# Kernel tuning notes

Measured on AMD Instinct MI355X. Metric: run time of the kernel, lower is better.

## Reference

```python
import jax, jax.numpy as jnp
import numpy as np
import math

B, T, L, C = 4, 8, 512, 768
H = 8
HD = C // H  # 96
EPS = 1e-12  # F.normalize eps


def _l2norm(x):
    # F.normalize(x, dim=-1): x / max(||x||2, eps)
    n = jnp.sqrt(jnp.sum(x * x, axis=-1, keepdims=True))
    return x / jnp.maximum(n, EPS)


def setup_inputs() -> dict:
    key = jax.random.key(0)
    ks = jax.random.split(key, 7)
    s = 1.0 / math.sqrt(C)
    x = jax.random.normal(ks[0], (B, T, L, C), dtype=jnp.float32)
    Wq = jax.random.uniform(ks[1], (C, C), jnp.float32, -s, s)
    bq = jax.random.uniform(ks[2], (C,), jnp.float32, -s, s)
    Wkv = jax.random.uniform(ks[3], (C, 2 * C), jnp.float32, -s, s)
    bkv = jax.random.uniform(ks[4], (2 * C,), jnp.float32, -s, s)
    Wm = jax.random.uniform(ks[5], (C, C), jnp.float32, -s, s)
    bm = jax.random.uniform(ks[6], (C,), jnp.float32, -s, s)
    return {"x": x, "Wq": Wq, "bq": bq, "Wkv": Wkv, "bkv": bkv, "Wm": Wm, "bm": bm}


def reference(x, Wq, bq, Wkv, bkv, Wm, bm):
    b, t, l, c = x.shape
    # q: (b,t,l,c) -> (b,t,H,l,hd), L2-normalized over hd
    q = (x @ Wq + bq).reshape(b, t, l, H, HD).transpose(0, 1, 3, 2, 4)
    q = _l2norm(q)
    # kv: (b,t,l,2c) -> (b,t,2H,l,hd); chunk on head axis -> k = heads [0,H), v = heads [H,2H)
    kv = (x @ Wkv + bkv).reshape(b, t, l, 2 * H, HD).transpose(0, 1, 3, 2, 4)
    k = _l2norm(kv[:, :, :H])
    v = _l2norm(kv[:, :, H:])
    # attention (dropout on scores is identity in eval mode)
    scores = jnp.einsum("bthqd,bthkd->bthqk", q, k) / math.sqrt(HD)
    attn = jax.nn.softmax(scores, axis=-1)
    out = jnp.einsum("bthqk,bthkd->bthqd", attn, v)
    # (b,t,H,l,hd) -> (b,t,l,c), output projection (drop2 identity in eval)
    out = out.transpose(0, 1, 3, 2, 4).reshape(b, t, l, c)
    return out @ Wm + bm
```

## Files before the change

### kernel.cpp

```cpp
#include <hip/hip_runtime.h>
#include <hip/hip_bf16.h>


typedef __attribute__((ext_vector_type(8))) short bf16x8;
typedef __attribute__((ext_vector_type(4))) float f32x4;
typedef __attribute__((ext_vector_type(4))) int int4v;

__device__ __forceinline__ float b2f(unsigned short u) {
    return __uint_as_float(((unsigned)u) << 16);
}
__device__ __forceinline__ unsigned short f2b(float f) {
    unsigned u = __float_as_uint(f);
    u = (u + 0x7fffu + ((u >> 16) & 1u)) >> 16;
    return (unsigned short)u;
}

__device__ __forceinline__ void gll16(const unsigned short* g, unsigned short* l) {
    __builtin_amdgcn_global_load_lds((const __attribute__((address_space(1))) unsigned int*)g,
                                     (__attribute__((address_space(3))) unsigned int*)l, 16, 0, 0);
}

#define VMCNT(n) asm volatile("s_waitcnt vmcnt(" #n ")" ::: "memory")
#define BAR()    __builtin_amdgcn_s_barrier()
#define SCHED0() __builtin_amdgcn_sched_barrier(0)
#define PRIO(x)  __builtin_amdgcn_s_setprio(x)

__global__ __launch_bounds__(256) void cast_bf16_k(const float* __restrict__ x,
                                                   unsigned short* __restrict__ xb, int n4) {
    int i = blockIdx.x * 256 + threadIdx.x;
    if (i >= n4) return;
    float4 v = ((const float4*)x)[i];
    ushort4 o;
    o.x = f2b(v.x); o.y = f2b(v.y); o.z = f2b(v.z); o.w = f2b(v.w);
    ((ushort4*)xb)[i] = o;
}

__global__ __launch_bounds__(256) void pack_w_k(const float* __restrict__ Wq,
                                                const float* __restrict__ Wkv,
                                                const float* __restrict__ Wm,
                                                unsigned short* __restrict__ Wt) {
    __shared__ float tile[64][65];
    const int tid = threadIdx.x;
    const int tn = blockIdx.x % 48;
    const int tk = blockIdx.x / 48;
    const int n0 = tn * 64, k0 = tk * 64;
    const float* src; int ldn, coff;
    if (n0 < 768)       { src = Wq;  ldn = 768;  coff = n0; }
    else if (n0 < 2304) { src = Wkv; ldn = 1536; coff = n0 - 768; }
    else                { src = Wm;  ldn = 768;  coff = n0 - 2304; }
    const int j = tid & 63;
    for (int i = tid >> 6; i < 64; i += 4)
        tile[i][j] = src[(k0 + i) * ldn + coff + j];
    __syncthreads();
    const int ii = tid & 63;
    for (int jj = tid >> 6; jj < 64; jj += 4)
        Wt[(long)(n0 + jj) * 768 + k0 + ii] = f2b(tile[ii][jj]);
}

template <int EPI>
__global__ __launch_bounds__(512, 4) void gemm_k(const unsigned short* __restrict__ A,
                                                 const unsigned short* __restrict__ Bt,
                                                 const float* __restrict__ bias0,
                                                 const float* __restrict__ bias1,
                                                 unsigned short* __restrict__ Cb,
                                                 float* __restrict__ Cf,
                                                 int N, int K, int nbn) {
    extern __shared__ unsigned short lds[];
    const int tid = threadIdx.x;
    const int lane = tid & 63, wid = tid >> 6;
    const int wm = wid >> 1, wn = wid & 1;
    const int l15 = lane & 15, g = lane >> 4;

    const int nwg = gridDim.x;
    const int wg = (blockIdx.x & 7) * (nwg >> 3) + (blockIdx.x >> 3);
    const int bm = wg / nbn, bn = wg % nbn;

    const unsigned short* gA = A  + (long)bm * 256 * K;
    const unsigned short* gB = Bt + (long)bn * 128 * K;

    const long sgoff = (long)(tid >> 2) * K + (long)(((tid & 3) ^ ((tid >> 3) & 3)) * 8);
    const int swoff = wid * 512;

#define STAGE_ALL(T, BUFO) do { \
        const long kb0 = (long)(T) * 32; \
        gll16(gB + sgoff + kb0, lds + (BUFO) + 8192 + swoff); \
        gll16(gA + sgoff + kb0, lds + (BUFO) + swoff); \
        gll16(gA + sgoff + kb0 + (long)128 * K, lds + (BUFO) + 4096 + swoff); \
    } while (0)

    const int slot8 = (g ^ ((l15 >> 1) & 3)) * 8;
    f32x4 acc[4][4] = {};
    const int nkt = K >> 5;

    STAGE_ALL(0, 0);
    STAGE_ALL(1, 12288);

    int cur = 0, nx1 = 12288, nx2 = 24576;
    for (int t = 0; t < nkt; ++t) {
        if (t < nkt - 1) { VMCNT(3); } else { VMCNT(0); }
        BAR(); SCHED0();
        if (t + 2 < nkt) STAGE_ALL(t + 2, nx2);

        bf16x8 af[4], bv[4];
#pragma unroll
        for (int mf = 0; mf < 4; mf++)
            af[mf] = *(const bf16x8*)&lds[cur + (wm * 64 + mf * 16 + l15) * 32 + slot8];
#pragma unroll
        for (int nf = 0; nf < 4; nf++)
            bv[nf] = *(const bf16x8*)&lds[cur + 8192 + (wn * 64 + nf * 16 + l15) * 32 + slot8];
        PRIO(1);
#pragma unroll
        for (int mf = 0; mf < 4; mf++)
#pragma unroll
            for (int nf = 0; nf < 4; nf++)
                acc[mf][nf] = __builtin_amdgcn_mfma_f32_16x16x32_bf16(af[mf], bv[nf], acc[mf][nf], 0, 0, 0);
        PRIO(0);
        const int tmp = cur; cur = nx1; nx1 = nx2; nx2 = tmp;
    }
#undef STAGE_ALL

    float bvv[4];
#pragma unroll
    for (int nf = 0; nf < 4; nf++) {
        const int col = bn * 128 + wn * 64 + nf * 16 + l15;
        bvv[nf] = (EPI == 0) ? ((col < 768) ? bias0[col] : bias1[col - 768]) : bias0[col];
    }
#pragma unroll
    for (int mf = 0; mf < 4; mf++) {
#pragma unroll
        for (int r = 0; r < 4; r++) {
            const long row = bm * 256 + wm * 64 + mf * 16 + g * 4 + r;
#pragma unroll
            for (int nf = 0; nf < 4; nf++) {
                const float v = acc[mf][nf][r] + bvv[nf];
                if (EPI == 0) {
                    const unsigned hh = f2b(v);
                    const unsigned oo = __shfl_xor((int)hh, 1);
                    if (!(lane & 1))
                        *(unsigned*)&Cb[row * N + bn * 128 + wn * 64 + nf * 16 + l15] =
                            (hh & 0xffffu) | (oo << 16);
                } else {
                    Cf[row * N + bn * 128 + wn * 64 + nf * 16 + l15] = v;
                }
            }
        }
    }
}

__global__ __launch_bounds__(256) void knvn_k(const unsigned short* __restrict__ qkv,
                                              float* __restrict__ kinv,
                                              float* __restrict__ vinv) {
    const int tid = threadIdx.x, lane = tid & 63, w = tid >> 6;
    const int s = blockIdx.x * 4 + w;
    const int row = s >> 3, h = s & 7;
    const unsigned short* pk = qkv + (long)row * 2304 + 768 + h * 96;
    float k0 = 0.f, k1 = 0.f, v0 = 0.f, v1 = 0.f;
    if (lane < 48) {
        unsigned a = *(const unsigned*)(pk + lane * 2);
        unsigned b = *(const unsigned*)(pk + 768 + lane * 2);
        k0 = b2f((unsigned short)(a & 0xffffu)); k1 = b2f((unsigned short)(a >> 16));
        v0 = b2f((unsigned short)(b & 0xffffu)); v1 = b2f((unsigned short)(b >> 16));
    }
    float sk = k0 * k0 + k1 * k1;
    float sv = v0 * v0 + v1 * v1;
#pragma unroll
    for (int m = 1; m < 64; m <<= 1) { sk += __shfl_xor(sk, m); sv += __shfl_xor(sv, m); }
    if (lane == 0) {
        kinv[h * 16384 + row] = 1.f / fmaxf(sqrtf(sk), 1e-12f);
        vinv[h * 16384 + row] = 1.f / fmaxf(sqrtf(sv), 1e-12f);
    }
}

__global__ __launch_bounds__(512, 2) void attn_k(const unsigned short* __restrict__ qkv,
                                                 const float* __restrict__ kinv,
                                                 const float* __restrict__ vinv,
                                                 unsigned short* __restrict__ obuf) {
    constexpr float SCALE = 0.1020620726159658f;
    __shared__ unsigned short Qs[128 * 104];
    __shared__ unsigned short Ks[64 * 104];
    __shared__ unsigned short Vt[96 * 72];
    __shared__ float kinv_s[2][64], vinv_s[2][64];

    const int tid = threadIdx.x, lane = tid & 63, w = tid >> 6;
    const int bid0 = blockIdx.x;
    const int bid = (bid0 & 7) * 128 + (bid0 >> 3);
    const int qt = bid & 3, h = (bid >> 2) & 7, bt = bid >> 5;
    const long rowbase = (long)bt * 512 * 2304 + h * 96;
    const int l15 = lane & 15;
    const int g = lane >> 4;
    const int ko = g * 8;

    for (int j = 0; j < 3; j++) {
        const int c = tid + j * 512;
        const int r = c / 12, d8 = (c % 12) * 8;
        *(int4v*)&Qs[r * 104 + d8] = *(const int4v*)&qkv[rowbase + (long)(qt * 128 + r) * 2304 + d8];
    }
    if (tid < 256) {
#pragma unroll
        for (int j = 0; j < 3; j++) {
            const int c = tid + j * 256;
            const int r = c / 12, d8 = (c % 12) * 8;
            *(int4v*)&Ks[r * 104 + d8] = *(const int4v*)&qkv[rowbase + 768 + (long)r * 2304 + d8];
        }
    } else {
#pragma unroll
        for (int j = 0; j < 3; j++) {
            const int c = (tid - 256) + j * 256;
            const int key = c & 63, d8 = (c >> 6) * 8;
            int4v vv = *(const int4v*)&qkv[rowbase + 1536 + (long)key * 2304 + d8];
            const unsigned short* vp = (const unsigned short*)&vv;
#pragma unroll
            for (int i = 0; i < 8; i++) Vt[(d8 + i) * 72 + key] = vp[i];
        }
    }
    if (tid < 64)       kinv_s[0][tid]      = kinv[h * 16384 + bt * 512 + tid];
    else if (tid < 128) vinv_s[0][tid - 64] = vinv[h * 16384 + bt * 512 + tid - 64];
    __syncthreads();

    bf16x8 qf[3];
#pragma unroll
    for (int ks = 0; ks < 3; ks++)
        qf[ks] = *(const bf16x8*)&Qs[(w * 16 + l15) * 104 + ks * 32 + ko];
    float ssq = 0.f;
#pragma unroll
    for (int ks = 0; ks < 3; ks++)
#pragma unroll
        for (int j = 0; j < 8; j++) {
            const float f = b2f((unsigned short)qf[ks][j]);
            ssq += f * f;
        }
    ssq += __shfl_xor(ssq, 16);
    ssq += __shfl_xor(ssq, 32);
    const float qs = SCALE / fmaxf(sqrtf(ssq), 1e-12f);

    float l_run = 0.f;
    f32x4 oacc[6] = {};

    for (int kt = 0; kt < 8; kt++) {
        const int cb = kt & 1, nb = cb ^ 1;

        int4v preg[3];
        float tn = 0.f;
        if (kt < 7) {
            if (tid < 256) {
                const long kb = rowbase + 768 + (long)((kt + 1) * 64) * 2304;
#pragma unroll
                for (int j = 0; j < 3; j++) {
                    const int c = tid + j * 256;
                    preg[j] = *(const int4v*)&qkv[kb + (long)(c / 12) * 2304 + (c % 12) * 8];
                }
            } else {
                const long vb = rowbase + 1536 + (long)((kt + 1) * 64) * 2304;
#pragma unroll
                for (int j = 0; j < 3; j++) {
                    const int c = (tid - 256) + j * 256;
                    preg[j] = *(const int4v*)&qkv[vb + (long)(c & 63) * 2304 + (c >> 6) * 8];
                }
            }
            if (tid < 64)       tn = kinv[h * 16384 + bt * 512 + (kt + 1) * 64 + tid];
            else if (tid < 128) tn = vinv[h * 16384 + bt * 512 + (kt + 1) * 64 + tid - 64];
        }

        f32x4 sacc[4] = {};
#pragma unroll
        for (int ks = 0; ks < 3; ks++) {
#pragma unroll
            for (int kf = 0; kf < 4; kf++) {
                bf16x8 af = *(const bf16x8*)&Ks[(kf * 16 + l15) * 104 + ks * 32 + ko];
                sacc[kf] = __builtin_amdgcn_mfma_f32_16x16x32_bf16(af, qf[ks], sacc[kf], 0, 0, 0);
            }
        }

        float p[16];
        float s = 0.f;
#pragma unroll
        for (int kf = 0; kf < 4; kf++)
#pragma unroll
            for (int r = 0; r < 4; r++) {
                const float pv = __expf(sacc[kf][r] * qs * kinv_s[cb][kf * 16 + g * 4 + r]);
                s += pv;
                p[kf * 4 + r] = pv * vinv_s[cb][kf * 16 + g * 4 + r];
            }
        s += __shfl_xor(s, 16);
        s += __shfl_xor(s, 32);
        l_run += s;

        {
            unsigned* prow = (unsigned*)&Qs[(w * 16 + l15) * 104];
#pragma unroll
            for (int kf = 0; kf < 4; kf++)
#pragma unroll
                for (int rp = 0; rp < 2; rp++) {
                    unsigned pk = (unsigned)f2b(p[kf * 4 + 2 * rp]) |
                                  ((unsigned)f2b(p[kf * 4 + 2 * rp + 1]) << 16);
                    prow[kf * 8 + g * 2 + rp] = pk;
                }
        }

#pragma unroll
        for (int ks = 0; ks < 2; ks++) {
            bf16x8 pa = *(const bf16x8*)&Qs[(w * 16 + l15) * 104 + ks * 32 + ko];
#pragma unroll
            for (int nf = 0; nf < 6; nf++) {
                bf16x8 vb = *(const bf16x8*)&Vt[(nf * 16 + l15) * 72 + ks * 32 + ko];
                oacc[nf] = __builtin_amdgcn_mfma_f32_16x16x32_bf16(pa, vb, oacc[nf], 0, 0, 0);
            }
        }
        __syncthreads();

        if (kt < 7) {
            if (tid < 256) {
#pragma unroll
                for (int j = 0; j < 3; j++) {
                    const int c = tid + j * 256;
                    *(int4v*)&Ks[(c / 12) * 104 + (c % 12) * 8] = preg[j];
                }
            } else {
#pragma unroll
                for (int j = 0; j < 3; j++) {
                    const int c = (tid - 256) + j * 256;
                    const int key = c & 63, d8 = (c >> 6) * 8;
                    const unsigned short* vp = (const unsigned short*)&preg[j];
#pragma unroll
                    for (int i = 0; i < 8; i++) Vt[(d8 + i) * 72 + key] = vp[i];
                }
            }
            if (tid < 64)       kinv_s[nb][tid]      = tn;
            else if (tid < 128) vinv_s[nb][tid - 64] = tn;
            __syncthreads();
        }
    }

    const float inv = 1.f / l_run;
    float invr[4];
#pragma unroll
    for (int r = 0; r < 4; r++) invr[r] = __shfl(inv, g * 4 + r);
#pragma unroll
    for (int r = 0; r < 4; r++) {
        const int row = w * 16 + g * 4 + r;
        const long gr = ((long)(bt * 512 + qt * 128 + row)) * 768 + h * 96;
#pragma unroll
        for (int nf = 0; nf < 6; nf++)
            obuf[gr + nf * 16 + l15] = f2b(oacc[nf][r] * invr[r]);
    }
}

extern "C" void kernel_launch(void* const* d_in, const int* in_sizes, int n_in,
                              void* d_out, int out_size, void* d_ws, size_t ws_size,
                              hipStream_t stream) {
    const float* x   = (const float*)d_in[0];
    const float* Wq  = (const float*)d_in[1];
    const float* bq  = (const float*)d_in[2];
    const float* Wkv = (const float*)d_in[3];
    const float* bkv = (const float*)d_in[4];
    const float* Wm  = (const float*)d_in[5];
    const float* bm  = (const float*)d_in[6];
    float* out = (float*)d_out;

    char* ws = (char*)d_ws;
    unsigned short* xb  = (unsigned short*)ws;
    float*          vinv = (float*)ws;
    float*          kinv = (float*)(ws + 524288);
    unsigned short* wt  = (unsigned short*)(ws + 25165824);
    unsigned short* qkv = (unsigned short*)(ws + 29884416);
    unsigned short* ob  = (unsigned short*)(ws + 105381888);

    static bool attr_set = false;
    if (!attr_set) {
        hipFuncSetAttribute((const void*)gemm_k<0>, hipFuncAttributeMaxDynamicSharedMemorySize, 73728);
        hipFuncSetAttribute((const void*)gemm_k<1>, hipFuncAttributeMaxDynamicSharedMemorySize, 73728);
        attr_set = true;
    }

    cast_bf16_k<<<dim3(12288), dim3(256), 0, stream>>>(x, xb, 3145728);
    pack_w_k<<<dim3(576), dim3(256), 0, stream>>>(Wq, Wkv, Wm, wt);
    gemm_k<0><<<dim3(1152), dim3(512), 73728, stream>>>(xb, wt, bq, bkv, qkv, nullptr, 2304, 768, 18);
    knvn_k<<<dim3(32768), dim3(256), 0, stream>>>(qkv, kinv, vinv);
    attn_k<<<dim3(1024), dim3(512), 0, stream>>>(qkv, kinv, vinv, ob);
    gemm_k<1><<<dim3(384), dim3(512), 73728, stream>>>(ob, wt + (long)2304 * 768, bm, nullptr, nullptr, out, 768, 768, 6);
}
```

Before: 198.8 us.

## Shrink attention blocks to 64 queries and use 128x128 GEMM for output projection

The attention kernel now runs 256-thread blocks covering 64 query rows, twice as many blocks. Q fragments are loaded straight from global into registers, P gets its own small LDS buffer, and the register-prefetched double-buffered K/V loads are replaced by plain synchronous reloads. This is meant to raise occupancy and parallelism, at the cost of losing load/compute overlap in the attention loop. The output projection moves to a new 128x128-tile GEMM with a triple-buffered direct-to-LDS pipeline, giving 768 blocks instead of 384 for better CU fill.

```diff
diff --git a/kernel.cpp b/kernel.cpp
--- a/kernel.cpp
+++ b/kernel.cpp
@@ -147,6 +147,80 @@
     }
 }
 
+__global__ __launch_bounds__(512, 6) void gemm128_k(const unsigned short* __restrict__ A,
+                                                    const unsigned short* __restrict__ Bt,
+                                                    const float* __restrict__ bias0,
+                                                    float* __restrict__ Cf,
+                                                    int N, int K, int nbn) {
+    extern __shared__ unsigned short lds[];
+    const int tid = threadIdx.x;
+    const int lane = tid & 63, wid = tid >> 6;
+    const int wm = wid >> 2, wn = wid & 3;
+    const int l15 = lane & 15, g = lane >> 4;
+
+    const int nwg = gridDim.x;
+    const int wg = (blockIdx.x & 7) * (nwg >> 3) + (blockIdx.x >> 3);
+    const int bm = wg / nbn, bn = wg % nbn;
+
+    const unsigned short* gA = A  + (long)bm * 128 * K;
+    const unsigned short* gB = Bt + (long)bn * 128 * K;
+
+    const long sgoff = (long)(tid >> 2) * K + (long)(((tid & 3) ^ ((tid >> 3) & 3)) * 8);
+    const int swoff = wid * 512;
+
+#define STAGE2(T, BUFO) do { \
+        const long kb0 = (long)(T) * 32; \
+        gll16(gB + sgoff + kb0, lds + (BUFO) + 4096 + swoff); \
+        gll16(gA + sgoff + kb0, lds + (BUFO) + swoff); \
+    } while (0)
+
+    const int slot8 = (g ^ ((l15 >> 1) & 3)) * 8;
+    f32x4 acc[4][2] = {};
+    const int nkt = K >> 5;
+
+    STAGE2(0, 0);
+    STAGE2(1, 8192);
+
+    int cur = 0, nx1 = 8192, nx2 = 16384;
+    for (int t = 0; t < nkt; ++t) {
+        if (t < nkt - 1) { VMCNT(2); } else { VMCNT(0); }
+        BAR(); SCHED0();
+        if (t + 2 < nkt) STAGE2(t + 2, nx2);
+
+        bf16x8 af[4], bv[2];
+#pragma unroll
+        for (int mf = 0; mf < 4; mf++)
+            af[mf] = *(const bf16x8*)&lds[cur + (wm * 64 + mf * 16 + l15) * 32 + slot8];
+#pragma unroll
+        for (int nf = 0; nf < 2; nf++)
+            bv[nf] = *(const bf16x8*)&lds[cur + 4096 + (wn * 32 + nf * 16 + l15) * 32 + slot8];
+        PRIO(1);
+#pragma unroll
+        for (int mf = 0; mf < 4; mf++)
+#pragma unroll
+            for (int nf = 0; nf < 2; nf++)
+                acc[mf][nf] = __builtin_amdgcn_mfma_f32_16x16x32_bf16(af[mf], bv[nf], acc[mf][nf], 0, 0, 0);
+        PRIO(0);
+        const int tmp = cur; cur = nx1; nx1 = nx2; nx2 = tmp;
+    }
+#undef STAGE2
+
+    float bvv[2];
+#pragma unroll
+    for (int nf = 0; nf < 2; nf++)
+        bvv[nf] = bias0[bn * 128 + wn * 32 + nf * 16 + l15];
+#pragma unroll
+    for (int mf = 0; mf < 4; mf++) {
+#pragma unroll
+        for (int r = 0; r < 4; r++) {
+            const long row = bm * 128 + wm * 64 + mf * 16 + g * 4 + r;
+#pragma unroll
+            for (int nf = 0; nf < 2; nf++)
+                Cf[row * N + bn * 128 + wn * 32 + nf * 16 + l15] = acc[mf][nf][r] + bvv[nf];
+        }
+    }
+}
+
 __global__ __launch_bounds__(256) void knvn_k(const unsigned short* __restrict__ qkv,
                                               float* __restrict__ kinv,
                                               float* __restrict__ vinv) {
@@ -171,56 +245,49 @@
     }
 }
 
-__global__ __launch_bounds__(512, 2) void attn_k(const unsigned short* __restrict__ qkv,
+__global__ __launch_bounds__(256, 4) void attn_k(const unsigned short* __restrict__ qkv,
                                                  const float* __restrict__ kinv,
                                                  const float* __restrict__ vinv,
                                                  unsigned short* __restrict__ obuf) {
     constexpr float SCALE = 0.1020620726159658f;
-    __shared__ unsigned short Qs[128 * 104];
+    __shared__ unsigned short Ps[64 * 72];
     __shared__ unsigned short Ks[64 * 104];
     __shared__ unsigned short Vt[96 * 72];
-    __shared__ float kinv_s[2][64], vinv_s[2][64];
+    __shared__ float kinv_s[64], vinv_s[64];
 
     const int tid = threadIdx.x, lane = tid & 63, w = tid >> 6;
     const int bid0 = blockIdx.x;
-    const int bid = (bid0 & 7) * 128 + (bid0 >> 3);
-    const int qt = bid & 3, h = (bid >> 2) & 7, bt = bid >> 5;
+    const int bid = (bid0 & 7) * 256 + (bid0 >> 3);
+    const int qt = bid & 7, h = (bid >> 3) & 7, bt = bid >> 6;
     const long rowbase = (long)bt * 512 * 2304 + h * 96;
     const int l15 = lane & 15;
     const int g = lane >> 4;
     const int ko = g * 8;
 
+    bf16x8 qf[3];
+    {
+        const unsigned short* qrow = qkv + rowbase + (long)(qt * 64 + w * 16 + l15) * 2304;
+#pragma unroll
+        for (int ks = 0; ks < 3; ks++)
+            qf[ks] = *(const bf16x8*)&qrow[ks * 32 + ko];
+    }
     for (int j = 0; j < 3; j++) {
-        const int c = tid + j * 512;
+        const int c = tid + j * 256;
         const int r = c / 12, d8 = (c % 12) * 8;
-        *(int4v*)&Qs[r * 104 + d8] = *(const int4v*)&qkv[rowbase + (long)(qt * 128 + r) * 2304 + d8];
-    }
-    if (tid < 256) {
-#pragma unroll
-        for (int j = 0; j < 3; j++) {
-            const int c = tid + j * 256;
-            const int r = c / 12, d8 = (c % 12) * 8;
-            *(int4v*)&Ks[r * 104 + d8] = *(const int4v*)&qkv[rowbase + 768 + (long)r * 2304 + d8];
-        }
-    } else {
-#pragma unroll
-        for (int j = 0; j < 3; j++) {
-            const int c = (tid - 256) + j * 256;
-            const int key = c & 63, d8 = (c >> 6) * 8;
-            int4v vv = *(const int4v*)&qkv[rowbase + 1536 + (long)key * 2304 + d8];
-            const unsigned short* vp = (const unsigned short*)&vv;
-#pragma unroll
-            for (int i = 0; i < 8; i++) Vt[(d8 + i) * 72 + key] = vp[i];
-        }
-    }
-    if (tid < 64)       kinv_s[0][tid]      = kinv[h * 16384 + bt * 512 + tid];
-    else if (tid < 128) vinv_s[0][tid - 64] = vinv[h * 16384 + bt * 512 + tid - 64];
+        *(int4v*)&Ks[r * 104 + d8] = *(const int4v*)&qkv[rowbase + 768 + (long)r * 2304 + d8];
+    }
+    for (int j = 0; j < 3; j++) {
+        const int c = tid + j * 256;
+        const int key = c & 63, d8 = (c >> 6) * 8;
+        int4v vv = *(const int4v*)&qkv[rowbase + 1536 + (long)key * 2304 + d8];
+        const unsigned short* vp = (const unsigned short*)&vv;
+#pragma unroll
+        for (int i = 0; i < 8; i++) Vt[(d8 + i) * 72 + key] = vp[i];
+    }
+    if (tid < 64)       kinv_s[tid]      = kinv[h * 16384 + bt * 512 + tid];
+    else if (tid < 128) vinv_s[tid - 64] = vinv[h * 16384 + bt * 512 + tid - 64];
     __syncthreads();
 
-    bf16x8 qf[3];
-#pragma unroll
-    for (int ks = 0; ks < 3; ks++)
-        qf[ks] = *(const bf16x8*)&Qs[(w * 16 + l15) * 104 + ks * 32 + ko];
     float ssq = 0.f;
 #pragma unroll
     for (int ks = 0; ks < 3; ks++)
@@ -237,30 +304,6 @@
     f32x4 oacc[6] = {};
 
     for (int kt = 0; kt < 8; kt++) {
-        const int cb = kt & 1, nb = cb ^ 1;
-
-        int4v preg[3];
-        float tn = 0.f;
-        if (kt < 7) {
-            if (tid < 256) {
-                const long kb = rowbase + 768 + (long)((kt + 1) * 64) * 2304;
-#pragma unroll
-                for (int j = 0; j < 3; j++) {
-                    const int c = tid + j * 256;
-                    preg[j] = *(const int4v*)&qkv[kb + (long)(c / 12) * 2304 + (c % 12) * 8];
-                }
-            } else {
-                const long vb = rowbase + 1536 + (long)((kt + 1) * 64) * 2304;
-#pragma unroll
-                for (int j = 0; j < 3; j++) {
-                    const int c = (tid - 256) + j * 256;
-                    preg[j] = *(const int4v*)&qkv[vb + (long)(c & 63) * 2304 + (c >> 6) * 8];
-                }
-            }
-            if (tid < 64)       tn = kinv[h * 16384 + bt * 512 + (kt + 1) * 64 + tid];
-            else if (tid < 128) tn = vinv[h * 16384 + bt * 512 + (kt + 1) * 64 + tid - 64];
-        }
-
         f32x4 sacc[4] = {};
 #pragma unroll
         for (int ks = 0; ks < 3; ks++) {
@@ -277,16 +320,16 @@
         for (int kf = 0; kf < 4; kf++)
 #pragma unroll
             for (int r = 0; r < 4; r++) {
-                const float pv = __expf(sacc[kf][r] * qs * kinv_s[cb][kf * 16 + g * 4 + r]);
+                const float pv = __expf(sacc[kf][r] * qs * kinv_s[kf * 16 + g * 4 + r]);
                 s += pv;
-                p[kf * 4 + r] = pv * vinv_s[cb][kf * 16 + g * 4 + r];
+                p[kf * 4 + r] = pv * vinv_s[kf * 16 + g * 4 + r];
             }
         s += __shfl_xor(s, 16);
         s += __shfl_xor(s, 32);
         l_run += s;
 
         {
-            unsigned* prow = (unsigned*)&Qs[(w * 16 + l15) * 104];
+            unsigned* prow = (unsigned*)&Ps[(w * 16 + l15) * 72];
 #pragma unroll
             for (int kf = 0; kf < 4; kf++)
 #pragma unroll
@@ -299,7 +342,7 @@
 
 #pragma unroll
         for (int ks = 0; ks < 2; ks++) {
-            bf16x8 pa = *(const bf16x8*)&Qs[(w * 16 + l15) * 104 + ks * 32 + ko];
+            bf16x8 pa = *(const bf16x8*)&Ps[(w * 16 + l15) * 72 + ks * 32 + ko];
 #pragma unroll
             for (int nf = 0; nf < 6; nf++) {
                 bf16x8 vb = *(const bf16x8*)&Vt[(nf * 16 + l15) * 72 + ks * 32 + ko];
@@ -309,24 +352,23 @@
         __syncthreads();
 
         if (kt < 7) {
-            if (tid < 256) {
-#pragma unroll
-                for (int j = 0; j < 3; j++) {
-                    const int c = tid + j * 256;
-                    *(int4v*)&Ks[(c / 12) * 104 + (c % 12) * 8] = preg[j];
-                }
-            } else {
-#pragma unroll
-                for (int j = 0; j < 3; j++) {
-                    const int c = (tid - 256) + j * 256;
-                    const int key = c & 63, d8 = (c >> 6) * 8;
-                    const unsigned short* vp = (const unsigned short*)&preg[j];
-#pragma unroll
-                    for (int i = 0; i < 8; i++) Vt[(d8 + i) * 72 + key] = vp[i];
-                }
-            }
-            if (tid < 64)       kinv_s[nb][tid]      = tn;
-            else if (tid < 128) vinv_s[nb][tid - 64] = tn;
+            const int kn = kt + 1;
+            for (int j = 0; j < 3; j++) {
+                const int c = tid + j * 256;
+                const int r = c / 12, d8 = (c % 12) * 8;
+                *(int4v*)&Ks[r * 104 + d8] =
+                    *(const int4v*)&qkv[rowbase + 768 + (long)(kn * 64 + r) * 2304 + d8];
+            }
+            for (int j = 0; j < 3; j++) {
+                const int c = tid + j * 256;
+                const int key = c & 63, d8 = (c >> 6) * 8;
+                int4v vv = *(const int4v*)&qkv[rowbase + 1536 + (long)(kn * 64 + key) * 2304 + d8];
+                const unsigned short* vp = (const unsigned short*)&vv;
+#pragma unroll
+                for (int i = 0; i < 8; i++) Vt[(d8 + i) * 72 + key] = vp[i];
+            }
+            if (tid < 64)       kinv_s[tid]      = kinv[h * 16384 + bt * 512 + kn * 64 + tid];
+            else if (tid < 128) vinv_s[tid - 64] = vinv[h * 16384 + bt * 512 + kn * 64 + tid - 64];
             __syncthreads();
         }
     }
@@ -338,7 +380,7 @@
 #pragma unroll
     for (int r = 0; r < 4; r++) {
         const int row = w * 16 + g * 4 + r;
-        const long gr = ((long)(bt * 512 + qt * 128 + row)) * 768 + h * 96;
+        const long gr = ((long)(bt * 512 + qt * 64 + row)) * 768 + h * 96;
 #pragma unroll
         for (int nf = 0; nf < 6; nf++)
             obuf[gr + nf * 16 + l15] = f2b(oacc[nf][r] * invr[r]);
@@ -368,7 +410,7 @@
     static bool attr_set = false;
     if (!attr_set) {
         hipFuncSetAttribute((const void*)gemm_k<0>, hipFuncAttributeMaxDynamicSharedMemorySize, 73728);
-        hipFuncSetAttribute((const void*)gemm_k<1>, hipFuncAttributeMaxDynamicSharedMemorySize, 73728);
+        hipFuncSetAttribute((const void*)gemm128_k, hipFuncAttributeMaxDynamicSharedMemorySize, 49152);
         attr_set = true;
     }
 
@@ -376,6 +418,6 @@
     pack_w_k<<<dim3(576), dim3(256), 0, stream>>>(Wq, Wkv, Wm, wt);
     gemm_k<0><<<dim3(1152), dim3(512), 73728, stream>>>(xb, wt, bq, bkv, qkv, nullptr, 2304, 768, 18);
     knvn_k<<<dim3(32768), dim3(256), 0, stream>>>(qkv, kinv, vinv);
-    attn_k<<<dim3(1024), dim3(512), 0, stream>>>(qkv, kinv, vinv, ob);
-    gemm_k<1><<<dim3(384), dim3(512), 73728, stream>>>(ob, wt + (long)2304 * 768, bm, nullptr, nullptr, out, 768, 768, 6);
-}
+    attn_k<<<dim3(2048), dim3(256), 0, stream>>>(qkv, kinv, vinv, ob);
+    gemm128_k<<<dim3(768), dim3(512), 49152, stream>>>(ob, wt + (long)2304 * 768, bm, out, 768, 768, 6);
+}
```

Result: slower. 204.8 us (+3.0%).
